# Kernel tuning notes

Hardware: AMD Instinct MI355X
Metric: run time of the kernel (lower is better)

The kernel has to match this reference:

```python
import jax, jax.numpy as jnp
import numpy as np

N = 65536; C = 128; NCLS = 10; K = 27
VOXEL = 0.04; THR = 0.15
BIAS_PRIOR = -4.59511985013459  # bias_init_with_prob(0.01)

def _bn_elu(x, g, b):
    # eval-mode MinkowskiBatchNorm folded into per-channel affine, then ELU
    return jax.nn.elu(x * g + b)

def _nconv(x, nbr, W):
    # sparse 3x3x3 Minkowski conv via precomputed 27-neighbor kernel map
    out = x[nbr[:, 0]] @ W[0]
    for k in range(1, K):
        out = out + x[nbr[:, k]] @ W[k]
    return out

def setup_inputs():
    key = jax.random.key(0)
    ks = jax.random.split(key, 32)
    r = lambda i, shape: jax.random.normal(ks[i], shape, jnp.float32) * 0.02
    ones = lambda shape: jnp.ones(shape, jnp.float32)
    zeros = lambda shape: jnp.zeros(shape, jnp.float32)
    return {
        "coords": jnp.concatenate([jnp.zeros((N, 1), jnp.int32),
                                   jax.random.randint(ks[0], (N, 3), 0, 400, dtype=jnp.int32)], axis=1),
        "feats": jax.random.normal(ks[1], (N, C), jnp.float32),
        "nbr": jax.random.randint(ks[2], (N, K), 0, N, dtype=jnp.int32),
        "Wsem": r(3, (C, NCLS)), "bsem": jnp.full((NCLS,), BIAS_PRIOR, jnp.float32),
        "off_w1": r(4, (C, C)), "off_g1": ones(C), "off_b1": zeros(C),
        "off_w2": r(5, (C, C)), "off_g2": ones(C), "off_b2": zeros(C),
        "off_w3": r(6, (C, 3)),
        "fo_w": r(7, (K, C, C)), "fo_g": ones(C), "fo_b": zeros(C),
        "cls_out_w": r(8, (NCLS, C, C)), "cls_out_g": ones((NCLS, C)), "cls_out_b": zeros((NCLS, C)),
        "up_w": r(9, (NCLS, C, C)), "up_g": ones((NCLS, C)), "up_b": zeros((NCLS, C)),
        "fuse_w": r(10, (NCLS, 2 * C, C)), "fuse_g": ones((NCLS, C)), "fuse_b": zeros((NCLS, C)),
        "exp_w": r(11, (NCLS, C, C)), "exp_g": ones((NCLS, C)), "exp_b": zeros((NCLS, C)),
        "ctr_w": r(12, (C, 1)), "reg_w": r(13, (C, 6)),
        "cls_w": r(14, (C, NCLS)), "cls_b": jnp.full((NCLS,), BIAS_PRIOR, jnp.float32),
        "scales": ones(NCLS),
    }

def reference(coords, feats, nbr, Wsem, bsem,
              off_w1, off_g1, off_b1, off_w2, off_g2, off_b2, off_w3,
              fo_w, fo_g, fo_b,
              cls_out_w, cls_out_g, cls_out_b,
              up_w, up_g, up_b,
              fuse_w, fuse_g, fuse_b,
              exp_w, exp_g, exp_b,
              ctr_w, reg_w, cls_w, cls_b, scales):
    xyz = coords[:, 1:].astype(jnp.float32) * VOXEL                 # [N,3] metric coords
    max_b = (coords[:, 1:].max(0) + 1).astype(jnp.float32) * VOXEL  # scene bounds (+stride)
    min_b = (coords[:, 1:].min(0) - 1).astype(jnp.float32) * VOXEL
    # semantic 1x1 conv
    sem = feats @ Wsem + bsem                                       # [N,NCLS]
    # offset block: 1x1 conv -> BN -> ELU (x2) -> 1x1 conv to 3
    h = _bn_elu(feats @ off_w1, off_g1, off_b1)
    h = _bn_elu(h @ off_w2, off_g2, off_b2)
    voxel_offsets = h @ off_w3                                      # [N,3]
    voted = jnp.clip(xyz + jax.lax.stop_gradient(voxel_offsets), min_b, max_b)  # voted coords (feed assigner/NMS)
    # feature_offset: 3x3x3 sparse conv -> BN -> ELU
    offset_features = _bn_elu(_nconv(feats, nbr, fo_w), fo_g, fo_b)  # [N,C]
    sem_prob = jax.lax.stop_gradient(jax.nn.sigmoid(sem))
    outs = []
    for c in range(NCLS):
        # per-class semantic gating (mask == torch.nonzero selection, static-shape form)
        mask = (sem_prob[:, c] > THR).astype(feats.dtype)            # [N]
        m2 = jnp.concatenate([mask, mask])[:, None]                  # voted + original point sets
        fuse_feats = jnp.concatenate([offset_features, feats], axis=0) * m2  # [2N,C]
        hc = _bn_elu(fuse_feats @ cls_out_w[c], cls_out_g[c], cls_out_b[c])
        uc = _bn_elu(hc @ up_w[c], up_g[c], up_b[c])                 # cls_individual_up
        fc = _bn_elu(jnp.concatenate([hc, uc], axis=-1) @ fuse_w[c], fuse_g[c], fuse_b[c])
        ec = _bn_elu(fc @ exp_w[c], exp_g[c], exp_b[c])              # cls_individual_expand_out
        ctr = ec @ ctr_w                                             # centerness logits [2N,1]
        reg = jnp.exp(scales[c] * (ec @ reg_w))                      # fcaf3d distance preds [2N,6]
        cls = ec @ cls_w + cls_b                                     # cls logits [2N,NCLS]
        outs.append(jnp.concatenate([ctr, reg, cls], axis=-1) * m2)
    del voted  # consumed by downstream assigner/NMS, not a head tensor output
    return jnp.stack(outs)  # [NCLS, 2N, 1+6+NCLS]
```

## Files before the change

kernel.cpp:

```cpp
#include <hip/hip_runtime.h>
#include <math.h>


#define NCH   128
#define NCLS_ 10
#define KNBR  27
#define THRV  0.15f

__device__ __forceinline__ float elu1(float x) {
    return x > 0.0f ? x : expm1f(x);
}

__global__ __launch_bounds__(256) void mask_kernel(
    const float* __restrict__ feats,
    const float* __restrict__ Wsem,
    const float* __restrict__ bsem,
    unsigned int* __restrict__ maskbits,
    int N)
{
    __shared__ float part[4][64][11];

    const int tid  = threadIdx.x;
    const int lane = tid & 63;
    const int w    = __builtin_amdgcn_readfirstlane(tid >> 6);
    const int r0   = blockIdx.x * 64;
    const int row  = r0 + lane;

    if (row < N) {
        const float* fp = feats + (size_t)row * NCH + w * 32;
        float fr[32];
#pragma unroll
        for (int k = 0; k < 8; ++k) {
            const float4 v = ((const float4*)fp)[k];
            fr[4 * k + 0] = v.x; fr[4 * k + 1] = v.y;
            fr[4 * k + 2] = v.z; fr[4 * k + 3] = v.w;
        }
        const float* wp = Wsem + (size_t)(w * 32) * NCLS_;
        float acc[NCLS_];
#pragma unroll
        for (int c = 0; c < NCLS_; ++c) acc[c] = 0.0f;
#pragma unroll
        for (int jj = 0; jj < 32; ++jj) {
            const float fv = fr[jj];
            const float* wrow = wp + jj * NCLS_;
#pragma unroll
            for (int c = 0; c < NCLS_; ++c) acc[c] += fv * wrow[c];
        }
#pragma unroll
        for (int c = 0; c < NCLS_; ++c) part[w][lane][c] = acc[c];
    }
    __syncthreads();

    if (tid < 64 && r0 + tid < N) {
        unsigned int bits = 0u;
#pragma unroll
        for (int c = 0; c < NCLS_; ++c) {
            const float s = part[0][tid][c] + part[1][tid][c]
                          + part[2][tid][c] + part[3][tid][c] + bsem[c];
            const float p = 1.0f / (1.0f + expf(-s));
            if (p > THRV) bits |= (1u << c);
        }
        maskbits[r0 + tid] = bits;
    }
}

__global__ __launch_bounds__(256) void chain_kernel(
    const float* __restrict__ feats, const int* __restrict__ nbr,
    const unsigned int* __restrict__ maskbits,
    const float* __restrict__ fo_w, const float* __restrict__ fo_g, const float* __restrict__ fo_b,
    const float* __restrict__ cls_out_w, const float* __restrict__ cls_out_g, const float* __restrict__ cls_out_b,
    const float* __restrict__ up_w, const float* __restrict__ up_g, const float* __restrict__ up_b,
    const float* __restrict__ fuse_w, const float* __restrict__ fuse_g, const float* __restrict__ fuse_b,
    const float* __restrict__ exp_w, const float* __restrict__ exp_g, const float* __restrict__ exp_b,
    const float* __restrict__ ctr_w, const float* __restrict__ reg_w,
    const float* __restrict__ cls_w, const float* __restrict__ cls_b,
    const float* __restrict__ scales,
    float* __restrict__ out, int N, int chunks)
{
    const int c     = blockIdx.x / chunks;
    const int chunk = blockIdx.x % chunks;
    const int i0    = chunk * 256;
    const int tid   = threadIdx.x;

    {
        const size_t base1 = ((size_t)c * 2 * N + i0) * 17;
        const size_t base2 = ((size_t)c * 2 * N + N + i0) * 17;
        float4 z4 = make_float4(0.f, 0.f, 0.f, 0.f);
        float4* p1 = (float4*)(out + base1);
        float4* p2 = (float4*)(out + base2);
        const int n4 = 256 * 17 / 4;
        for (int idx = tid; idx < n4; idx += 256) { p1[idx] = z4; p2[idx] = z4; }
    }

    __shared__ unsigned long long wball[4];
    {
        const unsigned int mb = maskbits[i0 + tid];
        const unsigned long long bal = __ballot(((mb >> c) & 1u) != 0u);
        if ((tid & 63) == 0) wball[tid >> 6] = bal;
    }
    __syncthreads();
    const unsigned long long any = wball[0] | wball[1] | wball[2] | wball[3];
    if (any == 0ULL) return;

    __shared__ float xs[NCH];
    __shared__ float xin[2][NCH];
    __shared__ float hbuf[2][NCH];
    __shared__ float ubuf[2][NCH];
    __shared__ float fbuf[2][NCH];
    __shared__ float ebuf[2][NCH];

    const int h = tid >> 7;
    const int t = tid & 127;

    for (int i = i0; i < i0 + 256; ++i) {
        const unsigned int bits = maskbits[i];
        if (!((bits >> c) & 1u)) continue;

        float acc = 0.0f;
        for (int k = 0; k < KNBR; ++k) {
            if (tid < NCH) {
                const int nb = nbr[(size_t)i * KNBR + k];
                xs[tid] = feats[(size_t)nb * NCH + tid];
            }
            __syncthreads();
            if (tid < NCH) {
                const float* Wk = fo_w + (size_t)k * NCH * NCH;
#pragma unroll 8
                for (int j = 0; j < NCH; ++j)
                    acc += xs[j] * Wk[j * NCH + tid];
            }
            __syncthreads();
        }
        if (tid < NCH) xin[0][tid] = elu1(acc * fo_g[tid] + fo_b[tid]);
        else           xin[1][t]   = feats[(size_t)i * NCH + t];
        __syncthreads();

        {
            const float* W = cls_out_w + (size_t)c * NCH * NCH;
            float v = 0.0f;
#pragma unroll 8
            for (int j = 0; j < NCH; ++j) v += xin[h][j] * W[j * NCH + t];
            v = elu1(v * cls_out_g[c * NCH + t] + cls_out_b[c * NCH + t]);
            hbuf[h][t] = v;
        }
        __syncthreads();
        {
            const float* W = up_w + (size_t)c * NCH * NCH;
            float v = 0.0f;
#pragma unroll 8
            for (int j = 0; j < NCH; ++j) v += hbuf[h][j] * W[j * NCH + t];
            v = elu1(v * up_g[c * NCH + t] + up_b[c * NCH + t]);
            ubuf[h][t] = v;
        }
        __syncthreads();
        {
            const float* W = fuse_w + (size_t)c * 2 * NCH * NCH;
            float v = 0.0f;
#pragma unroll 8
            for (int j = 0; j < NCH; ++j) v += hbuf[h][j] * W[j * NCH + t];
#pragma unroll 8
            for (int j = 0; j < NCH; ++j) v += ubuf[h][j] * W[(NCH + j) * NCH + t];
            v = elu1(v * fuse_g[c * NCH + t] + fuse_b[c * NCH + t]);
            fbuf[h][t] = v;
        }
        __syncthreads();
        {
            const float* W = exp_w + (size_t)c * NCH * NCH;
            float v = 0.0f;
#pragma unroll 8
            for (int j = 0; j < NCH; ++j) v += fbuf[h][j] * W[j * NCH + t];
            v = elu1(v * exp_g[c * NCH + t] + exp_b[c * NCH + t]);
            ebuf[h][t] = v;
        }
        __syncthreads();
        if (t < 17) {
            float a = 0.0f;
            if (t == 0) {
                for (int j = 0; j < NCH; ++j) a += ebuf[h][j] * ctr_w[j];
            } else if (t < 7) {
                const int r = t - 1;
                for (int j = 0; j < NCH; ++j) a += ebuf[h][j] * reg_w[j * 6 + r];
                a = expf(scales[c] * a);
            } else {
                const int q = t - 7;
                for (int j = 0; j < NCH; ++j) a += ebuf[h][j] * cls_w[j * NCLS_ + q];
                a += cls_b[q];
            }
            out[((size_t)c * 2 * N + (size_t)h * N + i) * 17 + t] = a;
        }
        __syncthreads();
    }
}

extern "C" void kernel_launch(void* const* d_in, const int* in_sizes, int n_in,
                              void* d_out, int out_size, void* d_ws, size_t ws_size,
                              hipStream_t stream) {
    const float* feats = (const float*)d_in[1];
    const int*   nbr   = (const int*)d_in[2];
    const float* Wsem  = (const float*)d_in[3];
    const float* bsem  = (const float*)d_in[4];
    const float* fo_w  = (const float*)d_in[12];
    const float* fo_g  = (const float*)d_in[13];
    const float* fo_b  = (const float*)d_in[14];
    const float* cls_out_w = (const float*)d_in[15];
    const float* cls_out_g = (const float*)d_in[16];
    const float* cls_out_b = (const float*)d_in[17];
    const float* up_w  = (const float*)d_in[18];
    const float* up_g  = (const float*)d_in[19];
    const float* up_b  = (const float*)d_in[20];
    const float* fuse_w = (const float*)d_in[21];
    const float* fuse_g = (const float*)d_in[22];
    const float* fuse_b = (const float*)d_in[23];
    const float* exp_w = (const float*)d_in[24];
    const float* exp_g = (const float*)d_in[25];
    const float* exp_b = (const float*)d_in[26];
    const float* ctr_w = (const float*)d_in[27];
    const float* reg_w = (const float*)d_in[28];
    const float* cls_w = (const float*)d_in[29];
    const float* cls_b = (const float*)d_in[30];
    const float* scales = (const float*)d_in[31];

    const int N = in_sizes[1] / NCH;
    unsigned int* maskbits = (unsigned int*)d_ws;
    float* out = (float*)d_out;

    const int chunks = N / 256;

    mask_kernel<<<dim3((N + 63) / 64), dim3(256), 0, stream>>>(
        feats, Wsem, bsem, maskbits, N);

    chain_kernel<<<dim3(NCLS_ * chunks), dim3(256), 0, stream>>>(
        feats, nbr, maskbits,
        fo_w, fo_g, fo_b,
        cls_out_w, cls_out_g, cls_out_b,
        up_w, up_g, up_b,
        fuse_w, fuse_g, fuse_b,
        exp_w, exp_g, exp_b,
        ctr_w, reg_w, cls_w, cls_b, scales,
        out, N, chunks);
}
```

Measured before the change: 186.8 us.

## Fuse semantic mask computation into chain kernel with per-block class loop

```diff
diff --git a/kernel.cpp b/kernel.cpp
--- a/kernel.cpp
+++ b/kernel.cpp
@@ -6,67 +6,15 @@
 #define NCLS_ 10
 #define KNBR  27
 #define THRV  0.15f
+#define ROWS  64
 
 __device__ __forceinline__ float elu1(float x) {
     return x > 0.0f ? x : expm1f(x);
 }
 
-__global__ __launch_bounds__(256) void mask_kernel(
-    const float* __restrict__ feats,
-    const float* __restrict__ Wsem,
-    const float* __restrict__ bsem,
-    unsigned int* __restrict__ maskbits,
-    int N)
-{
-    __shared__ float part[4][64][11];
-
-    const int tid  = threadIdx.x;
-    const int lane = tid & 63;
-    const int w    = __builtin_amdgcn_readfirstlane(tid >> 6);
-    const int r0   = blockIdx.x * 64;
-    const int row  = r0 + lane;
-
-    if (row < N) {
-        const float* fp = feats + (size_t)row * NCH + w * 32;
-        float fr[32];
-#pragma unroll
-        for (int k = 0; k < 8; ++k) {
-            const float4 v = ((const float4*)fp)[k];
-            fr[4 * k + 0] = v.x; fr[4 * k + 1] = v.y;
-            fr[4 * k + 2] = v.z; fr[4 * k + 3] = v.w;
-        }
-        const float* wp = Wsem + (size_t)(w * 32) * NCLS_;
-        float acc[NCLS_];
-#pragma unroll
-        for (int c = 0; c < NCLS_; ++c) acc[c] = 0.0f;
-#pragma unroll
-        for (int jj = 0; jj < 32; ++jj) {
-            const float fv = fr[jj];
-            const float* wrow = wp + jj * NCLS_;
-#pragma unroll
-            for (int c = 0; c < NCLS_; ++c) acc[c] += fv * wrow[c];
-        }
-#pragma unroll
-        for (int c = 0; c < NCLS_; ++c) part[w][lane][c] = acc[c];
-    }
-    __syncthreads();
-
-    if (tid < 64 && r0 + tid < N) {
-        unsigned int bits = 0u;
-#pragma unroll
-        for (int c = 0; c < NCLS_; ++c) {
-            const float s = part[0][tid][c] + part[1][tid][c]
-                          + part[2][tid][c] + part[3][tid][c] + bsem[c];
-            const float p = 1.0f / (1.0f + expf(-s));
-            if (p > THRV) bits |= (1u << c);
-        }
-        maskbits[r0 + tid] = bits;
-    }
-}
-
-__global__ __launch_bounds__(256) void chain_kernel(
+__global__ __launch_bounds__(256) void fused_kernel(
     const float* __restrict__ feats, const int* __restrict__ nbr,
-    const unsigned int* __restrict__ maskbits,
+    const float* __restrict__ Wsem, const float* __restrict__ bsem,
     const float* __restrict__ fo_w, const float* __restrict__ fo_g, const float* __restrict__ fo_b,
     const float* __restrict__ cls_out_w, const float* __restrict__ cls_out_g, const float* __restrict__ cls_out_b,
     const float* __restrict__ up_w, const float* __restrict__ up_g, const float* __restrict__ up_b,
@@ -75,32 +23,70 @@
     const float* __restrict__ ctr_w, const float* __restrict__ reg_w,
     const float* __restrict__ cls_w, const float* __restrict__ cls_b,
     const float* __restrict__ scales,
-    float* __restrict__ out, int N, int chunks)
+    float* __restrict__ out, int N)
 {
-    const int c     = blockIdx.x / chunks;
-    const int chunk = blockIdx.x % chunks;
-    const int i0    = chunk * 256;
-    const int tid   = threadIdx.x;
+    const int i0  = blockIdx.x * ROWS;
+    const int tid = threadIdx.x;
+
+    __shared__ float part[4][ROWS][11];
+    __shared__ unsigned int rowbits[ROWS];
+    __shared__ unsigned int anyword;
+
+    if (tid == 0) anyword = 0u;
 
     {
-        const size_t base1 = ((size_t)c * 2 * N + i0) * 17;
-        const size_t base2 = ((size_t)c * 2 * N + N + i0) * 17;
-        float4 z4 = make_float4(0.f, 0.f, 0.f, 0.f);
-        float4* p1 = (float4*)(out + base1);
-        float4* p2 = (float4*)(out + base2);
-        const int n4 = 256 * 17 / 4;
-        for (int idx = tid; idx < n4; idx += 256) { p1[idx] = z4; p2[idx] = z4; }
-    }
-
-    __shared__ unsigned long long wball[4];
+        const float4 z4 = make_float4(0.f, 0.f, 0.f, 0.f);
+#pragma unroll
+        for (int s = 0; s < 2 * NCLS_; ++s) {
+            const int c = s >> 1, h = s & 1;
+            float4* p = (float4*)(out + ((size_t)c * 2 * N + (size_t)h * N + i0) * 17);
+            for (int idx = tid; idx < ROWS * 17 / 4; idx += 256) p[idx] = z4;
+        }
+    }
+
     {
-        const unsigned int mb = maskbits[i0 + tid];
-        const unsigned long long bal = __ballot(((mb >> c) & 1u) != 0u);
-        if ((tid & 63) == 0) wball[tid >> 6] = bal;
+        const int lane = tid & 63;
+        const int w    = __builtin_amdgcn_readfirstlane(tid >> 6);
+        const int row  = i0 + lane;
+        const float* fp = feats + (size_t)row * NCH + w * 32;
+        float fr[32];
+#pragma unroll
+        for (int k = 0; k < 8; ++k) {
+            const float4 v = ((const float4*)fp)[k];
+            fr[4 * k + 0] = v.x; fr[4 * k + 1] = v.y;
+            fr[4 * k + 2] = v.z; fr[4 * k + 3] = v.w;
+        }
+        const float* wp = Wsem + (size_t)(w * 32) * NCLS_;
+        float acc[NCLS_];
+#pragma unroll
+        for (int c = 0; c < NCLS_; ++c) acc[c] = 0.0f;
+#pragma unroll
+        for (int jj = 0; jj < 32; ++jj) {
+            const float fv = fr[jj];
+            const float* wrow = wp + jj * NCLS_;
+#pragma unroll
+            for (int c = 0; c < NCLS_; ++c) acc[c] += fv * wrow[c];
+        }
+#pragma unroll
+        for (int c = 0; c < NCLS_; ++c) part[w][lane][c] = acc[c];
     }
     __syncthreads();
-    const unsigned long long any = wball[0] | wball[1] | wball[2] | wball[3];
-    if (any == 0ULL) return;
+
+    if (tid < ROWS) {
+        unsigned int bits = 0u;
+#pragma unroll
+        for (int c = 0; c < NCLS_; ++c) {
+            const float s = part[0][tid][c] + part[1][tid][c]
+                          + part[2][tid][c] + part[3][tid][c] + bsem[c];
+            const float p = 1.0f / (1.0f + expf(-s));
+            if (p > THRV) bits |= (1u << c);
+        }
+        rowbits[tid] = bits;
+        if (bits) atomicOr(&anyword, bits);
+    }
+    __syncthreads();
+    const unsigned int any = anyword;
+    if (any == 0u) return;
 
     __shared__ float xs[NCH];
     __shared__ float xin[2][NCH];
@@ -112,83 +98,86 @@
     const int h = tid >> 7;
     const int t = tid & 127;
 
-    for (int i = i0; i < i0 + 256; ++i) {
-        const unsigned int bits = maskbits[i];
-        if (!((bits >> c) & 1u)) continue;
-
-        float acc = 0.0f;
-        for (int k = 0; k < KNBR; ++k) {
-            if (tid < NCH) {
-                const int nb = nbr[(size_t)i * KNBR + k];
-                xs[tid] = feats[(size_t)nb * NCH + tid];
-            }
-            __syncthreads();
-            if (tid < NCH) {
-                const float* Wk = fo_w + (size_t)k * NCH * NCH;
-#pragma unroll 8
-                for (int j = 0; j < NCH; ++j)
-                    acc += xs[j] * Wk[j * NCH + tid];
-            }
-            __syncthreads();
-        }
-        if (tid < NCH) xin[0][tid] = elu1(acc * fo_g[tid] + fo_b[tid]);
-        else           xin[1][t]   = feats[(size_t)i * NCH + t];
-        __syncthreads();
-
-        {
-            const float* W = cls_out_w + (size_t)c * NCH * NCH;
-            float v = 0.0f;
-#pragma unroll 8
-            for (int j = 0; j < NCH; ++j) v += xin[h][j] * W[j * NCH + t];
-            v = elu1(v * cls_out_g[c * NCH + t] + cls_out_b[c * NCH + t]);
-            hbuf[h][t] = v;
-        }
-        __syncthreads();
-        {
-            const float* W = up_w + (size_t)c * NCH * NCH;
-            float v = 0.0f;
-#pragma unroll 8
-            for (int j = 0; j < NCH; ++j) v += hbuf[h][j] * W[j * NCH + t];
-            v = elu1(v * up_g[c * NCH + t] + up_b[c * NCH + t]);
-            ubuf[h][t] = v;
-        }
-        __syncthreads();
-        {
-            const float* W = fuse_w + (size_t)c * 2 * NCH * NCH;
-            float v = 0.0f;
-#pragma unroll 8
-            for (int j = 0; j < NCH; ++j) v += hbuf[h][j] * W[j * NCH + t];
-#pragma unroll 8
-            for (int j = 0; j < NCH; ++j) v += ubuf[h][j] * W[(NCH + j) * NCH + t];
-            v = elu1(v * fuse_g[c * NCH + t] + fuse_b[c * NCH + t]);
-            fbuf[h][t] = v;
-        }
-        __syncthreads();
-        {
-            const float* W = exp_w + (size_t)c * NCH * NCH;
-            float v = 0.0f;
-#pragma unroll 8
-            for (int j = 0; j < NCH; ++j) v += fbuf[h][j] * W[j * NCH + t];
-            v = elu1(v * exp_g[c * NCH + t] + exp_b[c * NCH + t]);
-            ebuf[h][t] = v;
-        }
-        __syncthreads();
-        if (t < 17) {
-            float a = 0.0f;
-            if (t == 0) {
-                for (int j = 0; j < NCH; ++j) a += ebuf[h][j] * ctr_w[j];
-            } else if (t < 7) {
-                const int r = t - 1;
-                for (int j = 0; j < NCH; ++j) a += ebuf[h][j] * reg_w[j * 6 + r];
-                a = expf(scales[c] * a);
-            } else {
-                const int q = t - 7;
-                for (int j = 0; j < NCH; ++j) a += ebuf[h][j] * cls_w[j * NCLS_ + q];
-                a += cls_b[q];
-            }
-            out[((size_t)c * 2 * N + (size_t)h * N + i) * 17 + t] = a;
-        }
-        __syncthreads();
+    for (int c = 0; c < NCLS_; ++c) {
+        if (!((any >> c) & 1u)) continue;
+        for (int r = 0; r < ROWS; ++r) {
+            if (!((rowbits[r] >> c) & 1u)) continue;
+            const int i = i0 + r;
+
+            float acc = 0.0f;
+            for (int k = 0; k < KNBR; ++k) {
+                if (tid < NCH) {
+                    const int nb = nbr[(size_t)i * KNBR + k];
+                    xs[tid] = feats[(size_t)nb * NCH + tid];
+                }
+                __syncthreads();
+                if (tid < NCH) {
+                    const float* Wk = fo_w + (size_t)k * NCH * NCH;
+#pragma unroll 8
+                    for (int j = 0; j < NCH; ++j)
+                        acc += xs[j] * Wk[j * NCH + tid];
+                }
+                __syncthreads();
+            }
+            if (tid < NCH) xin[0][tid] = elu1(acc * fo_g[tid] + fo_b[tid]);
+            else           xin[1][t]   = feats[(size_t)i * NCH + t];
+            __syncthreads();
+
+            {
+                const float* W = cls_out_w + (size_t)c * NCH * NCH;
+                float v = 0.0f;
+#pragma unroll 8
+                for (int j = 0; j < NCH; ++j) v += xin[h][j] * W[j * NCH + t];
+                v = elu1(v * cls_out_g[c * NCH + t] + cls_out_b[c * NCH + t]);
+                hbuf[h][t] = v;
+            }
+            __syncthreads();
+            {
+                const float* W = up_w + (size_t)c * NCH * NCH;
+                float v = 0.0f;
+#pragma unroll 8
+                for (int j = 0; j < NCH; ++j) v += hbuf[h][j] * W[j * NCH + t];
+                v = elu1(v * up_g[c * NCH + t] + up_b[c * NCH + t]);
+                ubuf[h][t] = v;
+            }
+            __syncthreads();
+            {
+                const float* W = fuse_w + (size_t)c * 2 * NCH * NCH;
+                float v = 0.0f;
+#pragma unroll 8
+                for (int j = 0; j < NCH; ++j) v += hbuf[h][j] * W[j * NCH + t];
+#pragma unroll 8
+                for (int j = 0; j < NCH; ++j) v += ubuf[h][j] * W[(NCH + j) * NCH + t];
+                v = elu1(v * fuse_g[c * NCH + t] + fuse_b[c * NCH + t]);
+                fbuf[h][t] = v;
+            }
+            __syncthreads();
+            {
+                const float* W = exp_w + (size_t)c * NCH * NCH;
+                float v = 0.0f;
+#pragma unroll 8
+                for (int j = 0; j < NCH; ++j) v += fbuf[h][j] * W[j * NCH + t];
+                v = elu1(v * exp_g[c * NCH + t] + exp_b[c * NCH + t]);
+                ebuf[h][t] = v;
+            }
+            __syncthreads();
+            if (t < 17) {
+                float a = 0.0f;
+                if (t == 0) {
+                    for (int j = 0; j < NCH; ++j) a += ebuf[h][j] * ctr_w[j];
+                } else if (t < 7) {
+                    const int rr = t - 1;
+                    for (int j = 0; j < NCH; ++j) a += ebuf[h][j] * reg_w[j * 6 + rr];
+                    a = expf(scales[c] * a);
+                } else {
+                    const int q = t - 7;
+                    for (int j = 0; j < NCH; ++j) a += ebuf[h][j] * cls_w[j * NCLS_ + q];
+                    a += cls_b[q];
+                }
+                out[((size_t)c * 2 * N + (size_t)h * N + i) * 17 + t] = a;
+            }
+            __syncthreads();
+        }
     }
 }
 
@@ -221,21 +210,15 @@
     const float* scales = (const float*)d_in[31];
 
     const int N = in_sizes[1] / NCH;
-    unsigned int* maskbits = (unsigned int*)d_ws;
     float* out = (float*)d_out;
 
-    const int chunks = N / 256;
-
-    mask_kernel<<<dim3((N + 63) / 64), dim3(256), 0, stream>>>(
-        feats, Wsem, bsem, maskbits, N);
-
-    chain_kernel<<<dim3(NCLS_ * chunks), dim3(256), 0, stream>>>(
-        feats, nbr, maskbits,
+    fused_kernel<<<dim3(N / ROWS), dim3(256), 0, stream>>>(
+        feats, nbr, Wsem, bsem,
         fo_w, fo_g, fo_b,
         cls_out_w, cls_out_g, cls_out_b,
         up_w, up_g, up_b,
         fuse_w, fuse_g, fuse_b,
         exp_w, exp_g, exp_b,
         ctr_w, reg_w, cls_w, cls_b, scales,
-        out, N, chunks);
+        out, N);
 }
```

Measured after the change: 185.2 us. About the same (-0.9%).
